# Kernel tuning notes

Hardware: AMD Instinct MI355X
Metric: run time of the kernel (lower is better)

## Reference

```python
import jax, jax.numpy as jnp
import numpy as np

H, D = 8, 16          # heads, per-head dim (hidden_channels=128)
HID = H * D
N = 200000            # movie nodes
E = 500000            # edges per metapath relation
IN = 256              # input feature dim
CLS = 3               # output classes


def setup_inputs() -> dict:
    key = jax.random.key(0)
    ks = jax.random.split(key, 13)
    return {
        "x_movie": jax.random.normal(ks[0], (N, IN), jnp.float32),
        "W_proj": jax.random.normal(ks[1], (IN, HID), jnp.float32) * 0.05,
        "b_proj": jnp.zeros((HID,), jnp.float32),
        "att_src0": jax.random.normal(ks[2], (H, D), jnp.float32) * 0.1,
        "att_dst0": jax.random.normal(ks[3], (H, D), jnp.float32) * 0.1,
        "att_src1": jax.random.normal(ks[4], (H, D), jnp.float32) * 0.1,
        "att_dst1": jax.random.normal(ks[5], (H, D), jnp.float32) * 0.1,
        "q": jax.random.normal(ks[6], (HID,), jnp.float32) * 0.1,
        "k_w": jax.random.normal(ks[7], (HID, HID), jnp.float32) * 0.05,
        "k_b": jnp.zeros((HID,), jnp.float32),
        "lin_w": jax.random.normal(ks[8], (HID, CLS), jnp.float32) * 0.05,
        "lin_b": jnp.zeros((CLS,), jnp.float32),
        "e0_src": jax.random.randint(ks[9], (E,), 0, N, jnp.int32),
        "e0_dst": jax.random.randint(ks[10], (E,), 0, N, jnp.int32),
        "e1_src": jax.random.randint(ks[11], (E,), 0, N, jnp.int32),
        "e1_dst": jax.random.randint(ks[12], (E,), 0, N, jnp.int32),
    }


def _han_rel(h, att_s, att_d, src, dst, n):
    # h: [N, H, D]; GAT-style per-relation attention with segment softmax over dst
    a_s = jnp.sum(h * att_s, axis=-1)                      # [N, H]
    a_d = jnp.sum(h * att_d, axis=-1)                      # [N, H]
    alpha = jax.nn.leaky_relu(a_s[src] + a_d[dst], 0.2)    # [E, H]
    m = jax.ops.segment_max(alpha, dst, num_segments=n)    # per-dst max
    ex = jnp.exp(alpha - m[dst])
    den = jax.ops.segment_sum(ex, dst, num_segments=n)
    w = ex / (den[dst] + 1e-16)                            # edge softmax (PyG eps)
    msg = (h[src] * w[:, :, None]).reshape(-1, HID)        # [E, HID]
    return jax.nn.relu(jax.ops.segment_sum(msg, dst, num_segments=n))


def reference(x_movie, W_proj, b_proj, att_src0, att_dst0, att_src1, att_dst1,
              q, k_w, k_b, lin_w, lin_b, e0_src, e0_dst, e1_src, e1_dst):
    # node-type projection (HANConv.proj), dropout omitted (eval mode)
    h = (x_movie @ W_proj + b_proj).reshape(-1, H, D)      # [N, H, D]
    out0 = _han_rel(h, att_src0, att_dst0, e0_src, e0_dst, N)  # [N, HID]
    out1 = _han_rel(h, att_src1, att_dst1, e1_src, e1_dst, N)
    # semantic-level attention (HANConv.group)
    outs = jnp.stack([out0, out1])                         # [M=2, N, HID]
    score = jnp.sum(jnp.tanh(outs @ k_w + k_b).mean(axis=1) * q, axis=-1)  # [M]
    beta = jax.nn.softmax(score)
    fused = jnp.einsum('m,mnf->nf', beta, outs)            # [N, HID]
    return fused @ lin_w + lin_b                           # [N, CLS]
```

## Files before the change

kernel.cpp:

```cpp
#include <hip/hip_runtime.h>


typedef __attribute__((ext_vector_type(8))) short bf16x8;
typedef __attribute__((ext_vector_type(4))) float f32x4;
typedef __attribute__((ext_vector_type(8))) unsigned short ushort8;

__device__ __forceinline__ unsigned short f2b(float f) {
  union { float f; unsigned u; } v; v.f = f;
  unsigned r = v.u + 0x7fffu + ((v.u >> 16) & 1u);
  return (unsigned short)(r >> 16);
}
__device__ __forceinline__ float b2f(unsigned short u) {
  union { unsigned u; float f; } v; v.u = ((unsigned)u) << 16;
  return v.f;
}
__device__ __forceinline__ float fast_tanh(float x) {
  x = fminf(fmaxf(x, -15.f), 15.f);
  float t = __expf(2.f * x);
  return 1.f - 2.f / (t + 1.f);
}
__device__ __forceinline__ void gload_lds16(const unsigned short* g, unsigned short* l) {
  __builtin_amdgcn_global_load_lds(
      (const __attribute__((address_space(1))) unsigned int*)g,
      (__attribute__((address_space(3))) unsigned int*)l, 16, 0, 0);
}

__global__ __launch_bounds__(256) void prep_kernel(
    const float* __restrict__ X, unsigned short* __restrict__ xb, int n,
    const int* __restrict__ e0d, const int* __restrict__ e1d,
    int* __restrict__ deg, int ne,
    const float* __restrict__ Wp, const float* __restrict__ kwm,
    unsigned short* __restrict__ Wpf, unsigned short* __restrict__ Kwf) {
  const int tid = threadIdx.x;
  int b = blockIdx.x;
  if (b < 1024) {
    const long total8 = (long)n * 32;
    for (long i = (long)b * 256 + tid; i < total8; i += 1024L * 256) {
      const float4* s = (const float4*)(X + i * 8);
      float4 v0 = s[0], v1 = s[1];
      ushort8 o;
      o[0] = f2b(v0.x); o[1] = f2b(v0.y); o[2] = f2b(v0.z); o[3] = f2b(v0.w);
      o[4] = f2b(v1.x); o[5] = f2b(v1.y); o[6] = f2b(v1.z); o[7] = f2b(v1.w);
      *(ushort8*)(xb + i * 8) = o;
    }
    return;
  }
  b -= 1024;
  const int cb = (2 * ne + 255) >> 8;
  if (b < cb) {
    int e = b * 256 + tid;
    if (e < ne) atomicAdd(&deg[e0d[e]], 1);
    else if (e < 2 * ne) atomicAdd(&deg[n + e1d[e - ne]], 1);
    return;
  }
  b -= cb;
  int t = b * 256 + tid;
  const float* W; unsigned short* Wf; int idx;
  if (t < 4096) { W = Wp; Wf = Wpf; idx = t; }
  else if (t < 6144) { W = kwm; Wf = Kwf; idx = t - 4096; }
  else return;
  int lane = idx & 63, nt = (idx >> 6) & 7, kt = idx >> 9;
  int c = lane & 15, ks = lane >> 4;
  int kbase = kt * 32 + ks * 8;
  int col = nt * 16 + c;
  ushort8 o;
#pragma unroll
  for (int j = 0; j < 8; ++j) o[j] = f2b(W[(size_t)(kbase + j) * 128 + col]);
  *(ushort8*)(Wf + (size_t)idx * 8) = o;
}

__global__ __launch_bounds__(256) void proj_mfma(
    const unsigned short* __restrict__ xb, const unsigned short* __restrict__ Wf,
    const float* __restrict__ bias,
    const float* __restrict__ as0v, const float* __restrict__ ad0v,
    const float* __restrict__ as1v, const float* __restrict__ ad1v,
    unsigned short* __restrict__ Hb, float* __restrict__ preb, int n) {
  __shared__ unsigned short ats[32768];
  const int tid = threadIdx.x;
  const int wid = tid >> 6, lane = tid & 63;
  const int wm = wid >> 1, wn = wid & 1;
  const int row0 = blockIdx.x * 128;
  const int r = lane & 15, ks = lane >> 4;

  {
    unsigned short* dstbase = ats + wid * 8192;
#pragma unroll
    for (int i = 0; i < 16; ++i) {
      int chunk = i * 64 + lane;
      int row = wid * 32 + (chunk >> 5);
      int c = chunk & 31;
      int grow = row0 + row;
      grow = grow < n ? grow : n - 1;
      const unsigned short* src = xb + (size_t)grow * 256 + ((c ^ (row & 7)) * 8);
      gload_lds16(src, dstbase + i * 512);
    }
  }
  __syncthreads();

  f32x4 acc[4][4] = {};
  const unsigned short* bptr = Wf + ((size_t)(wn * 4) * 64 + lane) * 8;
#pragma unroll
  for (int kt = 0; kt < 8; ++kt) {
    bf16x8 a[4], b[4];
#pragma unroll
    for (int mi = 0; mi < 4; ++mi) {
      int row = wm * 64 + mi * 16 + r;
      a[mi] = *(const bf16x8*)&ats[row * 256 + (((kt * 4 + ks) ^ (row & 7)) * 8)];
    }
#pragma unroll
    for (int ni = 0; ni < 4; ++ni)
      b[ni] = *(const bf16x8*)(bptr + ((size_t)kt * 8 + ni) * 512);
#pragma unroll
    for (int mi = 0; mi < 4; ++mi)
#pragma unroll
      for (int ni = 0; ni < 4; ++ni)
        acc[mi][ni] = __builtin_amdgcn_mfma_f32_16x16x32_bf16(a[mi], b[ni], acc[mi][ni], 0, 0, 0);
  }
  __syncthreads();

#pragma unroll
  for (int ni = 0; ni < 4; ++ni) {
    const int col = wn * 64 + ni * 16 + r;
    const float bv = bias[col];
#pragma unroll
    for (int mi = 0; mi < 4; ++mi)
#pragma unroll
      for (int i = 0; i < 4; ++i)
        ats[(wm * 64 + mi * 16 + ks * 4 + i) * 136 + col] = f2b(acc[mi][ni][i] + bv);
  }
  __syncthreads();

  {
    int row = tid >> 1, half = tid & 1;
    int grow = row0 + row;
    if (grow < n) {
      ushort8* dst = (ushort8*)(Hb + (size_t)grow * 128 + half * 64);
#pragma unroll
      for (int j = 0; j < 8; ++j) dst[j] = *(ushort8*)&ats[row * 136 + half * 64 + j * 8];
    }
  }

  const size_t n8 = (size_t)n * 8;
  for (int rh = tid; rh < 1024; rh += 256) {
    int row = rh >> 3, head = rh & 7;
    int node = row0 + row;
    if (node < n) {
      float hv[16];
#pragma unroll
      for (int j = 0; j < 16; ++j) hv[j] = b2f(ats[row * 136 + head * 16 + j]);
      float s0 = 0, d0 = 0, s1 = 0, d1 = 0;
      const float* p0 = as0v + head * 16;
      const float* p1 = ad0v + head * 16;
      const float* p2 = as1v + head * 16;
      const float* p3 = ad1v + head * 16;
#pragma unroll
      for (int j = 0; j < 16; ++j) {
        float v = hv[j];
        s0 += v * p0[j]; d0 += v * p1[j];
        s1 += v * p2[j]; d1 += v * p3[j];
      }
      size_t idx = (size_t)node * 8 + head;
      preb[idx] = s0;
      preb[n8 + idx] = d0;
      preb[2 * n8 + idx] = s1;
      preb[3 * n8 + idx] = d1;
    }
  }
}

__global__ __launch_bounds__(256) void scan1_kernel(
    const int* __restrict__ deg, int* __restrict__ pre, int* __restrict__ bsum, int m) {
  __shared__ int sd[256];
  int t = threadIdx.x;
  int base = blockIdx.x * 2048 + t * 8;
  int v[8], sum = 0;
#pragma unroll
  for (int j = 0; j < 8; ++j) {
    v[j] = (base + j < m) ? deg[base + j] : 0;
    sum += v[j];
  }
  sd[t] = sum;
  __syncthreads();
  for (int off = 1; off < 256; off <<= 1) {
    int x = (t >= off) ? sd[t - off] : 0;
    __syncthreads();
    if (t >= off) sd[t] += x;
    __syncthreads();
  }
  if (t == 255) bsum[blockIdx.x] = sd[255];
  int run = sd[t] - sum;
#pragma unroll
  for (int j = 0; j < 8; ++j) {
    if (base + j < m) pre[base + j] = run;
    run += v[j];
  }
}

__global__ __launch_bounds__(256) void scan2_kernel(int* __restrict__ bsum, int nb) {
  __shared__ int sd[256];
  int t = threadIdx.x;
  int v = (t < nb) ? bsum[t] : 0;
  sd[t] = v;
  __syncthreads();
  for (int off = 1; off < 256; off <<= 1) {
    int x = (t >= off) ? sd[t - off] : 0;
    __syncthreads();
    if (t >= off) sd[t] += x;
    __syncthreads();
  }
  if (t < nb) bsum[t] = sd[t] - v;
}

__global__ void scan3_kernel(int* __restrict__ pre, const int* __restrict__ bsum, int m, int total) {
  int i = blockIdx.x * 256 + threadIdx.x;
  if (i < m) pre[i] += bsum[i >> 11];
  if (i == m) pre[m] = total;
}

__global__ void fill2_kernel(const int* __restrict__ e0s, const int* __restrict__ e0d,
                             const int* __restrict__ e1s, const int* __restrict__ e1d,
                             const int* __restrict__ pre, int* __restrict__ cur,
                             int* __restrict__ csr, int ne, int n) {
  int e = blockIdx.x * 256 + threadIdx.x;
  int s, idx;
  if (e < ne) { idx = e0d[e]; s = e0s[e]; }
  else if (e < 2 * ne) { idx = n + e1d[e - ne]; s = e1s[e - ne]; }
  else return;
  int slot = pre[idx] + atomicAdd(&cur[idx], 1);
  csr[slot] = s;
}

__global__ __launch_bounds__(256) void agg2_kernel(
    const int* __restrict__ pre, const int* __restrict__ csr,
    const unsigned short* __restrict__ Hb, const float* __restrict__ preb,
    unsigned short* __restrict__ outb, int n) {
  int rel = blockIdx.y;
  int gid = blockIdx.x * 256 + threadIdx.x;
  int node = gid >> 5;
  int lane = gid & 31;
  if (node >= n) return;
  int head = lane >> 2;
  const size_t n8 = (size_t)n * 8;
  const float* a_s = preb + (size_t)(2 * rel) * n8;
  const float* a_d = preb + (size_t)(2 * rel + 1) * n8;
  int beg = pre[rel * n + node], end = pre[rel * n + node + 1];
  float ad = a_d[(size_t)node * 8 + head];
  float s = 0.f;
  float ax = 0.f, ay = 0.f, az = 0.f, aw = 0.f;
  int e = beg;
  for (; e + 1 < end; e += 2) {
    int s0 = csr[e], s1 = csr[e + 1];
    float al0 = a_s[(size_t)s0 * 8 + head] + ad;
    float al1 = a_s[(size_t)s1 * 8 + head] + ad;
    ushort4 h0 = *(const ushort4*)(Hb + (size_t)s0 * 128 + lane * 4);
    ushort4 h1 = *(const ushort4*)(Hb + (size_t)s1 * 128 + lane * 4);
    al0 = (al0 >= 0.f) ? al0 : 0.2f * al0;
    al1 = (al1 >= 0.f) ? al1 : 0.2f * al1;
    float p0 = __expf(al0), p1 = __expf(al1);
    s += p0 + p1;
    ax += p0 * b2f(h0.x) + p1 * b2f(h1.x);
    ay += p0 * b2f(h0.y) + p1 * b2f(h1.y);
    az += p0 * b2f(h0.z) + p1 * b2f(h1.z);
    aw += p0 * b2f(h0.w) + p1 * b2f(h1.w);
  }
  if (e < end) {
    int s0 = csr[e];
    float al0 = a_s[(size_t)s0 * 8 + head] + ad;
    ushort4 h0 = *(const ushort4*)(Hb + (size_t)s0 * 128 + lane * 4);
    al0 = (al0 >= 0.f) ? al0 : 0.2f * al0;
    float p0 = __expf(al0);
    s += p0;
    ax += p0 * b2f(h0.x);
    ay += p0 * b2f(h0.y);
    az += p0 * b2f(h0.z);
    aw += p0 * b2f(h0.w);
  }
  float inv = 1.f / (s + 1e-16f);
  ushort4 o;
  o.x = f2b(fmaxf(ax * inv, 0.f));
  o.y = f2b(fmaxf(ay * inv, 0.f));
  o.z = f2b(fmaxf(az * inv, 0.f));
  o.w = f2b(fmaxf(aw * inv, 0.f));
  *(ushort4*)(outb + (size_t)rel * n * 128 + (size_t)node * 128 + lane * 4) = o;
}

__global__ __launch_bounds__(256) void score2_mfma(
    const unsigned short* __restrict__ outb, const unsigned short* __restrict__ Kf,
    const float* __restrict__ kb, const float* __restrict__ q,
    const float* __restrict__ lw, float* __restrict__ pout,
    float* __restrict__ sb, int n) {
  __shared__ unsigned short at[16384];
  __shared__ float red[256];
  const int rel = blockIdx.y;
  const unsigned short* A = outb + (size_t)rel * n * 128;
  const int tid = threadIdx.x;
  const int wid = tid >> 6, lane = tid & 63;
  const int wm = wid >> 1, wn = wid & 1;
  const int row0 = blockIdx.x * 128;
  const int r = lane & 15, ks = lane >> 4;

  {
    unsigned short* dstbase = at + wid * 4096;
#pragma unroll
    for (int i = 0; i < 8; ++i) {
      int chunk = i * 64 + lane;
      int row = wid * 32 + (chunk >> 4);
      int c = chunk & 15;
      int grow = row0 + row;
      grow = grow < n ? grow : n - 1;
      const unsigned short* src = A + (size_t)grow * 128 + ((c ^ (row & 7)) * 8);
      gload_lds16(src, dstbase + i * 512);
    }
  }
  __syncthreads();

  f32x4 acc[4][4] = {};
  const unsigned short* bptr = Kf + ((size_t)(wn * 4) * 64 + lane) * 8;
#pragma unroll
  for (int kt = 0; kt < 4; ++kt) {
    bf16x8 a[4], b[4];
#pragma unroll
    for (int mi = 0; mi < 4; ++mi) {
      int row = wm * 64 + mi * 16 + r;
      a[mi] = *(const bf16x8*)&at[row * 128 + (((kt * 4 + ks) ^ (row & 7)) * 8)];
    }
#pragma unroll
    for (int ni = 0; ni < 4; ++ni)
      b[ni] = *(const bf16x8*)(bptr + ((size_t)kt * 8 + ni) * 512);
#pragma unroll
    for (int mi = 0; mi < 4; ++mi)
#pragma unroll
      for (int ni = 0; ni < 4; ++ni)
        acc[mi][ni] = __builtin_amdgcn_mfma_f32_16x16x32_bf16(a[mi], b[ni], acc[mi][ni], 0, 0, 0);
  }

  if (tid < 128) {
    int node = row0 + tid;
    if (node < n) {
      float p0 = 0.f, p1 = 0.f, p2 = 0.f;
      int s = tid & 7;
#pragma unroll
      for (int c = 0; c < 16; ++c) {
        const unsigned short* rp = &at[tid * 128 + ((c ^ s) * 8)];
#pragma unroll
        for (int j = 0; j < 8; ++j) {
          float v = b2f(rp[j]);
          const float* w = lw + (size_t)(c * 8 + j) * 3;
          p0 += v * w[0]; p1 += v * w[1]; p2 += v * w[2];
        }
      }
      float4 o = make_float4(p0, p1, p2, 0.f);
      *(float4*)(pout + (size_t)node * 8 + rel * 4) = o;
    }
  }

  float part = 0.f;
#pragma unroll
  for (int ni = 0; ni < 4; ++ni) {
    const int col = wn * 64 + ni * 16 + r;
    const float kbv = kb[col], qv = q[col];
#pragma unroll
    for (int mi = 0; mi < 4; ++mi) {
#pragma unroll
      for (int i = 0; i < 4; ++i) {
        int row = row0 + wm * 64 + mi * 16 + ks * 4 + i;
        if (row < n) part += fast_tanh(acc[mi][ni][i] + kbv) * qv;
      }
    }
  }
  red[tid] = part;
  __syncthreads();
  for (int off = 128; off > 0; off >>= 1) {
    if (tid < off) red[tid] += red[tid + off];
    __syncthreads();
  }
  if (tid == 0) atomicAdd(&sb[rel], red[0]);
}

__global__ void beta_kernel(float* __restrict__ sb, float invn) {
  if (threadIdx.x == 0 && blockIdx.x == 0) {
    float s0 = sb[0] * invn, s1 = sb[1] * invn;
    float m = fmaxf(s0, s1);
    float e0 = __expf(s0 - m), e1 = __expf(s1 - m);
    float d = e0 + e1;
    sb[2] = e0 / d;
    sb[3] = e1 / d;
  }
}

__global__ __launch_bounds__(256) void final2_kernel(
    const float* __restrict__ pout, const float* __restrict__ sb,
    const float* __restrict__ lb, float* __restrict__ out, int n) {
  int node = blockIdx.x * 256 + threadIdx.x;
  if (node >= n) return;
  float b0 = sb[2], b1 = sb[3];
  const float4* p = (const float4*)(pout + (size_t)node * 8);
  float4 pa = p[0], pb = p[1];
  float* d = out + (size_t)node * 3;
  d[0] = b0 * pa.x + b1 * pb.x + lb[0];
  d[1] = b0 * pa.y + b1 * pb.y + lb[1];
  d[2] = b0 * pa.z + b1 * pb.z + lb[2];
}

extern "C" void kernel_launch(void* const* d_in, const int* in_sizes, int n_in,
                              void* d_out, int out_size, void* d_ws, size_t ws_size,
                              hipStream_t stream) {
  const float* x   = (const float*)d_in[0];
  const float* Wp  = (const float*)d_in[1];
  const float* bp  = (const float*)d_in[2];
  const float* as0 = (const float*)d_in[3];
  const float* ad0 = (const float*)d_in[4];
  const float* as1 = (const float*)d_in[5];
  const float* ad1 = (const float*)d_in[6];
  const float* q   = (const float*)d_in[7];
  const float* kw  = (const float*)d_in[8];
  const float* kb  = (const float*)d_in[9];
  const float* lw  = (const float*)d_in[10];
  const float* lb  = (const float*)d_in[11];
  const int* e0s = (const int*)d_in[12];
  const int* e0d = (const int*)d_in[13];
  const int* e1s = (const int*)d_in[14];
  const int* e1d = (const int*)d_in[15];
  const int n  = in_sizes[0] / 256;
  const int ne = in_sizes[12];
  float* out = (float*)d_out;

  char* ws = (char*)d_ws;
  size_t off = 0;
  auto alloc = [&](size_t b) -> char* {
    char* p = ws + off;
    off = (off + b + 255) & ~(size_t)255;
    return p;
  };
  unsigned short* xb   = (unsigned short*)alloc((size_t)n * 256 * 2);
  unsigned short* h    = (unsigned short*)alloc((size_t)n * 128 * 2);
  unsigned short* outb = (unsigned short*)alloc((size_t)2 * n * 128 * 2);
  float* preb = (float*)alloc((size_t)4 * n * 8 * 4);
  float* pout = (float*)alloc((size_t)n * 8 * 4);
  int* pre    = (int*)alloc((size_t)(2 * n + 1) * 4);
  int* csr    = (int*)alloc((size_t)2 * ne * 4);
  int* deg    = (int*)alloc(((size_t)4 * n + 4) * 4);
  int* cur    = deg + 2 * n;
  float* sb   = (float*)(deg + 4 * n);
  int* bsum   = (int*)alloc(256 * 4);
  unsigned short* Wpf = (unsigned short*)alloc((size_t)4096 * 8 * 2);
  unsigned short* Kwf = (unsigned short*)alloc((size_t)2048 * 8 * 2);

  const int m = 2 * n;
  const int nblk_scan = (m + 2047) / 2048;
  const int cnt_blks = (2 * ne + 255) / 256;

  hipMemsetAsync(deg, 0, ((size_t)4 * n + 4) * 4, stream);
  hipLaunchKernelGGL(prep_kernel, dim3(1024 + cnt_blks + 24), dim3(256), 0, stream,
                     x, xb, n, e0d, e1d, deg, ne, Wp, kw, Wpf, Kwf);

  const int gproj = (n + 127) / 128;
  hipLaunchKernelGGL(proj_mfma, dim3(gproj), dim3(256), 0, stream,
                     xb, Wpf, bp, as0, ad0, as1, ad1, h, preb, n);

  hipLaunchKernelGGL(scan1_kernel, dim3(nblk_scan), dim3(256), 0, stream, deg, pre, bsum, m);
  hipLaunchKernelGGL(scan2_kernel, dim3(1), dim3(256), 0, stream, bsum, nblk_scan);
  hipLaunchKernelGGL(scan3_kernel, dim3((m + 1 + 255) / 256), dim3(256), 0, stream,
                     pre, bsum, m, 2 * ne);
  hipLaunchKernelGGL(fill2_kernel, dim3((2 * ne + 255) / 256), dim3(256), 0, stream,
                     e0s, e0d, e1s, e1d, pre, cur, csr, ne, n);
  hipLaunchKernelGGL(agg2_kernel, dim3((n * 32 + 255) / 256, 2), dim3(256), 0, stream,
                     pre, csr, h, preb, outb, n);

  hipLaunchKernelGGL(score2_mfma, dim3(gproj, 2), dim3(256), 0, stream,
                     outb, Kwf, kb, q, lw, pout, sb, n);
  hipLaunchKernelGGL(beta_kernel, dim3(1), dim3(64), 0, stream, sb, 1.0f / n);
  hipLaunchKernelGGL(final2_kernel, dim3((n + 255) / 256), dim3(256), 0, stream,
                     pout, sb, lb, out, n);
}
```

Before: 361.4 us.

## Fuse fp32-to-bf16 input conversion into projection GEMM and widen aggregation lanes

```diff
diff --git a/kernel.cpp b/kernel.cpp
--- a/kernel.cpp
+++ b/kernel.cpp
@@ -19,33 +19,19 @@
   float t = __expf(2.f * x);
   return 1.f - 2.f / (t + 1.f);
 }
-__device__ __forceinline__ void gload_lds16(const unsigned short* g, unsigned short* l) {
+__device__ __forceinline__ void gload_lds16(const void* g, void* l) {
   __builtin_amdgcn_global_load_lds(
       (const __attribute__((address_space(1))) unsigned int*)g,
       (__attribute__((address_space(3))) unsigned int*)l, 16, 0, 0);
 }
 
-__global__ __launch_bounds__(256) void prep_kernel(
-    const float* __restrict__ X, unsigned short* __restrict__ xb, int n,
+__global__ __launch_bounds__(256) void prep_lite(
     const int* __restrict__ e0d, const int* __restrict__ e1d,
-    int* __restrict__ deg, int ne,
+    int* __restrict__ deg, int ne, int n,
     const float* __restrict__ Wp, const float* __restrict__ kwm,
     unsigned short* __restrict__ Wpf, unsigned short* __restrict__ Kwf) {
   const int tid = threadIdx.x;
   int b = blockIdx.x;
-  if (b < 1024) {
-    const long total8 = (long)n * 32;
-    for (long i = (long)b * 256 + tid; i < total8; i += 1024L * 256) {
-      const float4* s = (const float4*)(X + i * 8);
-      float4 v0 = s[0], v1 = s[1];
-      ushort8 o;
-      o[0] = f2b(v0.x); o[1] = f2b(v0.y); o[2] = f2b(v0.z); o[3] = f2b(v0.w);
-      o[4] = f2b(v1.x); o[5] = f2b(v1.y); o[6] = f2b(v1.z); o[7] = f2b(v1.w);
-      *(ushort8*)(xb + i * 8) = o;
-    }
-    return;
-  }
-  b -= 1024;
   const int cb = (2 * ne + 255) >> 8;
   if (b < cb) {
     int e = b * 256 + tid;
@@ -70,84 +56,92 @@
 }
 
 __global__ __launch_bounds__(256) void proj_mfma(
-    const unsigned short* __restrict__ xb, const unsigned short* __restrict__ Wf,
+    const float* __restrict__ X, const unsigned short* __restrict__ Wf,
     const float* __restrict__ bias,
     const float* __restrict__ as0v, const float* __restrict__ ad0v,
     const float* __restrict__ as1v, const float* __restrict__ ad1v,
     unsigned short* __restrict__ Hb, float* __restrict__ preb, int n) {
-  __shared__ unsigned short ats[32768];
+  __shared__ float atsf[16384];
   const int tid = threadIdx.x;
   const int wid = tid >> 6, lane = tid & 63;
   const int wm = wid >> 1, wn = wid & 1;
-  const int row0 = blockIdx.x * 128;
+  const int row0 = blockIdx.x * 64;
   const int r = lane & 15, ks = lane >> 4;
 
   {
-    unsigned short* dstbase = ats + wid * 8192;
+    float* dstbase = atsf + wid * 16 * 256;
 #pragma unroll
     for (int i = 0; i < 16; ++i) {
-      int chunk = i * 64 + lane;
-      int row = wid * 32 + (chunk >> 5);
-      int c = chunk & 31;
+      int row = wid * 16 + i;
       int grow = row0 + row;
       grow = grow < n ? grow : n - 1;
-      const unsigned short* src = xb + (size_t)grow * 256 + ((c ^ (row & 7)) * 8);
-      gload_lds16(src, dstbase + i * 512);
-    }
-  }
-  __syncthreads();
-
-  f32x4 acc[4][4] = {};
+      const float* src = X + (size_t)grow * 256 + ((lane ^ (i & 7)) * 4);
+      gload_lds16(src, dstbase + i * 256);
+    }
+  }
+  __syncthreads();
+
+  f32x4 acc[2][4] = {};
   const unsigned short* bptr = Wf + ((size_t)(wn * 4) * 64 + lane) * 8;
+  const int sw = r & 7;
 #pragma unroll
   for (int kt = 0; kt < 8; ++kt) {
-    bf16x8 a[4], b[4];
-#pragma unroll
-    for (int mi = 0; mi < 4; ++mi) {
-      int row = wm * 64 + mi * 16 + r;
-      a[mi] = *(const bf16x8*)&ats[row * 256 + (((kt * 4 + ks) ^ (row & 7)) * 8)];
+    const int c0 = kt * 8 + ks * 2;
+    bf16x8 a[2], b[4];
+#pragma unroll
+    for (int mi = 0; mi < 2; ++mi) {
+      const float* lrow = atsf + (wm * 32 + mi * 16 + r) * 256;
+      float4 f0 = *(const float4*)(lrow + ((c0 ^ sw) * 4));
+      float4 f1 = *(const float4*)(lrow + (((c0 + 1) ^ sw) * 4));
+      bf16x8 v;
+      v[0] = (short)f2b(f0.x); v[1] = (short)f2b(f0.y);
+      v[2] = (short)f2b(f0.z); v[3] = (short)f2b(f0.w);
+      v[4] = (short)f2b(f1.x); v[5] = (short)f2b(f1.y);
+      v[6] = (short)f2b(f1.z); v[7] = (short)f2b(f1.w);
+      a[mi] = v;
     }
 #pragma unroll
     for (int ni = 0; ni < 4; ++ni)
       b[ni] = *(const bf16x8*)(bptr + ((size_t)kt * 8 + ni) * 512);
 #pragma unroll
-    for (int mi = 0; mi < 4; ++mi)
+    for (int mi = 0; mi < 2; ++mi)
 #pragma unroll
       for (int ni = 0; ni < 4; ++ni)
         acc[mi][ni] = __builtin_amdgcn_mfma_f32_16x16x32_bf16(a[mi], b[ni], acc[mi][ni], 0, 0, 0);
   }
   __syncthreads();
 
+  unsigned short* ct = (unsigned short*)atsf;
 #pragma unroll
   for (int ni = 0; ni < 4; ++ni) {
     const int col = wn * 64 + ni * 16 + r;
     const float bv = bias[col];
 #pragma unroll
-    for (int mi = 0; mi < 4; ++mi)
+    for (int mi = 0; mi < 2; ++mi)
 #pragma unroll
       for (int i = 0; i < 4; ++i)
-        ats[(wm * 64 + mi * 16 + ks * 4 + i) * 136 + col] = f2b(acc[mi][ni][i] + bv);
+        ct[(wm * 32 + mi * 16 + ks * 4 + i) * 136 + col] = f2b(acc[mi][ni][i] + bv);
   }
   __syncthreads();
 
   {
-    int row = tid >> 1, half = tid & 1;
+    int row = tid >> 2, qq = tid & 3;
     int grow = row0 + row;
     if (grow < n) {
-      ushort8* dst = (ushort8*)(Hb + (size_t)grow * 128 + half * 64);
-#pragma unroll
-      for (int j = 0; j < 8; ++j) dst[j] = *(ushort8*)&ats[row * 136 + half * 64 + j * 8];
+      ushort8* dst = (ushort8*)(Hb + (size_t)grow * 128 + qq * 32);
+#pragma unroll
+      for (int j = 0; j < 4; ++j) dst[j] = *(ushort8*)&ct[row * 136 + qq * 32 + j * 8];
     }
   }
 
   const size_t n8 = (size_t)n * 8;
-  for (int rh = tid; rh < 1024; rh += 256) {
+  for (int rh = tid; rh < 512; rh += 256) {
     int row = rh >> 3, head = rh & 7;
     int node = row0 + row;
     if (node < n) {
       float hv[16];
 #pragma unroll
-      for (int j = 0; j < 16; ++j) hv[j] = b2f(ats[row * 136 + head * 16 + j]);
+      for (int j = 0; j < 16; ++j) hv[j] = b2f(ct[row * 136 + head * 16 + j]);
       float s0 = 0, d0 = 0, s1 = 0, d1 = 0;
       const float* p0 = as0v + head * 16;
       const float* p1 = ad0v + head * 16;
@@ -236,52 +230,59 @@
     unsigned short* __restrict__ outb, int n) {
   int rel = blockIdx.y;
   int gid = blockIdx.x * 256 + threadIdx.x;
-  int node = gid >> 5;
-  int lane = gid & 31;
+  int node = gid >> 3;
+  int lane = gid & 7;
   if (node >= n) return;
-  int head = lane >> 2;
   const size_t n8 = (size_t)n * 8;
   const float* a_s = preb + (size_t)(2 * rel) * n8;
   const float* a_d = preb + (size_t)(2 * rel + 1) * n8;
   int beg = pre[rel * n + node], end = pre[rel * n + node + 1];
-  float ad = a_d[(size_t)node * 8 + head];
+  float ad = a_d[(size_t)node * 8 + lane];
   float s = 0.f;
-  float ax = 0.f, ay = 0.f, az = 0.f, aw = 0.f;
+  float acc[16] = {};
   int e = beg;
   for (; e + 1 < end; e += 2) {
     int s0 = csr[e], s1 = csr[e + 1];
-    float al0 = a_s[(size_t)s0 * 8 + head] + ad;
-    float al1 = a_s[(size_t)s1 * 8 + head] + ad;
-    ushort4 h0 = *(const ushort4*)(Hb + (size_t)s0 * 128 + lane * 4);
-    ushort4 h1 = *(const ushort4*)(Hb + (size_t)s1 * 128 + lane * 4);
+    float al0 = a_s[(size_t)s0 * 8 + lane] + ad;
+    float al1 = a_s[(size_t)s1 * 8 + lane] + ad;
+    const ushort8* h0p = (const ushort8*)(Hb + (size_t)s0 * 128 + lane * 16);
+    const ushort8* h1p = (const ushort8*)(Hb + (size_t)s1 * 128 + lane * 16);
+    ushort8 h0a = h0p[0], h0b = h0p[1];
+    ushort8 h1a = h1p[0], h1b = h1p[1];
     al0 = (al0 >= 0.f) ? al0 : 0.2f * al0;
     al1 = (al1 >= 0.f) ? al1 : 0.2f * al1;
     float p0 = __expf(al0), p1 = __expf(al1);
     s += p0 + p1;
-    ax += p0 * b2f(h0.x) + p1 * b2f(h1.x);
-    ay += p0 * b2f(h0.y) + p1 * b2f(h1.y);
-    az += p0 * b2f(h0.z) + p1 * b2f(h1.z);
-    aw += p0 * b2f(h0.w) + p1 * b2f(h1.w);
+#pragma unroll
+    for (int j = 0; j < 8; ++j) {
+      acc[j]     += p0 * b2f(h0a[j]) + p1 * b2f(h1a[j]);
+      acc[8 + j] += p0 * b2f(h0b[j]) + p1 * b2f(h1b[j]);
+    }
   }
   if (e < end) {
     int s0 = csr[e];
-    float al0 = a_s[(size_t)s0 * 8 + head] + ad;
-    ushort4 h0 = *(const ushort4*)(Hb + (size_t)s0 * 128 + lane * 4);
+    float al0 = a_s[(size_t)s0 * 8 + lane] + ad;
+    const ushort8* h0p = (const ushort8*)(Hb + (size_t)s0 * 128 + lane * 16);
+    ushort8 h0a = h0p[0], h0b = h0p[1];
     al0 = (al0 >= 0.f) ? al0 : 0.2f * al0;
     float p0 = __expf(al0);
     s += p0;
-    ax += p0 * b2f(h0.x);
-    ay += p0 * b2f(h0.y);
-    az += p0 * b2f(h0.z);
-    aw += p0 * b2f(h0.w);
+#pragma unroll
+    for (int j = 0; j < 8; ++j) {
+      acc[j]     += p0 * b2f(h0a[j]);
+      acc[8 + j] += p0 * b2f(h0b[j]);
+    }
   }
   float inv = 1.f / (s + 1e-16f);
-  ushort4 o;
-  o.x = f2b(fmaxf(ax * inv, 0.f));
-  o.y = f2b(fmaxf(ay * inv, 0.f));
-  o.z = f2b(fmaxf(az * inv, 0.f));
-  o.w = f2b(fmaxf(aw * inv, 0.f));
-  *(ushort4*)(outb + (size_t)rel * n * 128 + (size_t)node * 128 + lane * 4) = o;
+  ushort8 o0, o1;
+#pragma unroll
+  for (int j = 0; j < 8; ++j) {
+    o0[j] = f2b(fmaxf(acc[j] * inv, 0.f));
+    o1[j] = f2b(fmaxf(acc[8 + j] * inv, 0.f));
+  }
+  ushort8* dst = (ushort8*)(outb + (size_t)rel * n * 128 + (size_t)node * 128 + lane * 16);
+  dst[0] = o0;
+  dst[1] = o1;
 }
 
 __global__ __launch_bounds__(256) void score2_mfma(
@@ -432,7 +433,6 @@
     off = (off + b + 255) & ~(size_t)255;
     return p;
   };
-  unsigned short* xb   = (unsigned short*)alloc((size_t)n * 256 * 2);
   unsigned short* h    = (unsigned short*)alloc((size_t)n * 128 * 2);
   unsigned short* outb = (unsigned short*)alloc((size_t)2 * n * 128 * 2);
   float* preb = (float*)alloc((size_t)4 * n * 8 * 4);
@@ -451,12 +451,12 @@
   const int cnt_blks = (2 * ne + 255) / 256;
 
   hipMemsetAsync(deg, 0, ((size_t)4 * n + 4) * 4, stream);
-  hipLaunchKernelGGL(prep_kernel, dim3(1024 + cnt_blks + 24), dim3(256), 0, stream,
-                     x, xb, n, e0d, e1d, deg, ne, Wp, kw, Wpf, Kwf);
-
-  const int gproj = (n + 127) / 128;
+  hipLaunchKernelGGL(prep_lite, dim3(cnt_blks + 24), dim3(256), 0, stream,
+                     e0d, e1d, deg, ne, n, Wp, kw, Wpf, Kwf);
+
+  const int gproj = (n + 63) / 64;
   hipLaunchKernelGGL(proj_mfma, dim3(gproj), dim3(256), 0, stream,
-                     xb, Wpf, bp, as0, ad0, as1, ad1, h, preb, n);
+                     x, Wpf, bp, as0, ad0, as1, ad1, h, preb, n);
 
   hipLaunchKernelGGL(scan1_kernel, dim3(nblk_scan), dim3(256), 0, stream, deg, pre, bsum, m);
   hipLaunchKernelGGL(scan2_kernel, dim3(1), dim3(256), 0, stream, bsum, nblk_scan);
@@ -464,10 +464,10 @@
                      pre, bsum, m, 2 * ne);
   hipLaunchKernelGGL(fill2_kernel, dim3((2 * ne + 255) / 256), dim3(256), 0, stream,
                      e0s, e0d, e1s, e1d, pre, cur, csr, ne, n);
-  hipLaunchKernelGGL(agg2_kernel, dim3((n * 32 + 255) / 256, 2), dim3(256), 0, stream,
+  hipLaunchKernelGGL(agg2_kernel, dim3((n * 8 + 255) / 256, 2), dim3(256), 0, stream,
                      pre, csr, h, preb, outb, n);
 
-  hipLaunchKernelGGL(score2_mfma, dim3(gproj, 2), dim3(256), 0, stream,
+  hipLaunchKernelGGL(score2_mfma, dim3((n + 127) / 128, 2), dim3(256), 0, stream,
                      outb, Kwf, kb, q, lw, pout, sb, n);
   hipLaunchKernelGGL(beta_kernel, dim3(1), dim3(64), 0, stream, sb, 1.0f / n);
   hipLaunchKernelGGL(final2_kernel, dim3((n + 255) / 256), dim3(256), 0, stream,
```

Result: faster. 350.5 us (-3.0%).
